# Kernel tuning notes

Hardware: AMD Instinct MI355X
Metric: run time of the kernel (lower is better)

The kernel has to match this reference:

```python
import jax, jax.numpy as jnp
import numpy as np
import math

D_MODEL = 1024
N_HEADS = 16
HEAD_DIM = D_MODEL // N_HEADS
B = 2
S = 2048

def setup_inputs() -> dict:
    key = jax.random.key(0)
    ks = jax.random.split(key, 5)
    x = jax.random.normal(ks[0], (B, S, D_MODEL), dtype=jnp.float32)
    # causal lower-triangular mask, broadcastable to [B, H, S, S]
    mask = jnp.tril(jnp.ones((S, S), dtype=bool))[None, None, :, :]
    # qkv_proj: Linear(d_model, 3*d_model); out_proj: Linear(d_model, d_model)
    lim_qkv = 1.0 / math.sqrt(D_MODEL)
    Wqkv = jax.random.uniform(ks[1], (D_MODEL, 3 * D_MODEL), minval=-lim_qkv, maxval=lim_qkv, dtype=jnp.float32)
    bqkv = jax.random.uniform(ks[2], (3 * D_MODEL,), minval=-lim_qkv, maxval=lim_qkv, dtype=jnp.float32)
    Wo = jax.random.uniform(ks[3], (D_MODEL, D_MODEL), minval=-lim_qkv, maxval=lim_qkv, dtype=jnp.float32)
    bo = jax.random.uniform(ks[4], (D_MODEL,), minval=-lim_qkv, maxval=lim_qkv, dtype=jnp.float32)
    return {"x": x, "mask": mask, "Wqkv": Wqkv, "bqkv": bqkv, "Wo": Wo, "bo": bo}

def reference(x, mask, Wqkv, bqkv, Wo, bo):
    b, s, d = x.shape
    scale = math.sqrt(HEAD_DIM)
    qkv = x @ Wqkv + bqkv                                   # [b, s, 3d]
    qkv = qkv.reshape(b, s, 3, N_HEADS, HEAD_DIM)
    qkv = jnp.transpose(qkv, (2, 0, 3, 1, 4))               # [3, b, h, s, hd]
    q, k, v = qkv[0], qkv[1], qkv[2]
    scores = jnp.einsum("bhqd,bhkd->bhqk", q, k) / scale    # [b, h, s, s]
    scores = jnp.where(mask, scores, -jnp.inf)
    attn = jax.nn.softmax(scores, axis=-1)                  # dropout inactive (eval)
    out = jnp.einsum("bhqk,bhkd->bhqd", attn, v)            # [b, h, s, hd]
    out = jnp.transpose(out, (0, 2, 1, 3)).reshape(b, s, d)
    return out @ Wo + bo
```

## Files before the change

kernel.cpp:

```cpp
#include <hip/hip_runtime.h>
#include <stdint.h>

typedef __bf16 bf16x8 __attribute__((ext_vector_type(8)));
typedef float  f32x4  __attribute__((ext_vector_type(4)));

__device__ __forceinline__ float bf2f(ushort u) {
    union { uint i; float f; } v; v.i = ((uint)u) << 16; return v.f;
}
__device__ __forceinline__ ushort f2bf(float f) {
    union { uint i; float f; } v; v.f = f;
    uint i = v.i;
    uint r = (i + 0x7fffu + ((i >> 16) & 1u)) >> 16;
    return (ushort)r;
}
__device__ __forceinline__ ushort f2bf_t(float f) {
    union { uint i; float f; } v; v.f = f;
    return (ushort)(v.i >> 16);
}

#if __has_builtin(__builtin_amdgcn_exp2f)
#define EXP2F __builtin_amdgcn_exp2f
#else
#define EXP2F exp2f
#endif

__device__ __forceinline__ void gld16(const ushort* g, ushort* l) {
    __builtin_amdgcn_global_load_lds((const __attribute__((address_space(1))) uint*)g,
                                     (__attribute__((address_space(3))) uint*)l, 16, 0, 0);
}

#define D_MODEL 1024
#define N_HEADS 16
#define HEAD_DIM 64
#define BATCH 2
#define SEQ 2048
#define M_ROWS (BATCH * SEQ)
#define N_ITEMS 1024
#define SCALE_LOG2E 0.18033688f

__global__ __launch_bounds__(256) void cast_f32_bf16(
    const float* __restrict__ in, ushort* __restrict__ out, int n4)
{
    int i = blockIdx.x * 256 + threadIdx.x;
    if (i < n4) {
        float4 v = ((const float4*)in)[i];
        ushort4 o;
        o.x = f2bf(v.x); o.y = f2bf(v.y); o.z = f2bf(v.z); o.w = f2bf(v.w);
        ((ushort4*)out)[i] = o;
    }
}

__global__ __launch_bounds__(256) void transpose_f32_bf16(
    const float* __restrict__ in, ushort* __restrict__ out, int K, int N)
{
    __shared__ float tile[64][65];
    const int k0 = blockIdx.y << 6, n0 = blockIdx.x << 6;
    const int tid = threadIdx.x;
    {
        const int r  = tid >> 4;
        const int c4 = (tid & 15) * 4;
#pragma unroll
        for (int rr = 0; rr < 4; ++rr) {
            int kk = r + rr * 16;
            float4 v = *(const float4*)(in + (size_t)(k0 + kk) * N + n0 + c4);
            tile[kk][c4 + 0] = v.x; tile[kk][c4 + 1] = v.y;
            tile[kk][c4 + 2] = v.z; tile[kk][c4 + 3] = v.w;
        }
    }
    __syncthreads();
    {
        const int nn = tid & 63;
        const int ch = tid >> 6;
#pragma unroll
        for (int cc = 0; cc < 2; ++cc) {
            int k8 = (ch + cc * 4) * 8;
            ushort tmp[8] __attribute__((aligned(16)));
#pragma unroll
            for (int j = 0; j < 8; ++j) tmp[j] = f2bf(tile[k8 + j][nn]);
            *(uint4*)(out + (size_t)(n0 + nn) * K + k0 + k8) = *(const uint4*)tmp;
        }
    }
}

__global__ __launch_bounds__(256) void gemm_bt128(
    const ushort* __restrict__ A, const ushort* __restrict__ Bt,
    const float* __restrict__ bias, float* __restrict__ out,
    ushort* __restrict__ Qb, ushort* __restrict__ Kb, ushort* __restrict__ Vb,
    int M, int N, int K, int mode)
{
    __shared__ ushort smem[64 * 136];
    ushort* As = smem;
    ushort* Bs = smem + 128 * 32;
    const int tid = threadIdx.x, lane = tid & 63, w = tid >> 6;
    const int wr = w >> 1, wc = w & 1;
    const int m0 = blockIdx.y * 128, n0 = blockIdx.x * 128;
    const int quad = lane >> 4, r15 = lane & 15, q8 = quad * 8;

    f32x4 acc[4][4] = {};

    const int cb0 = w * 64;
    const int cb1 = 256 + w * 64;
    const int c0 = cb0 + lane, c1 = cb1 + lane;
    const int row0 = c0 >> 2, sc0 = (c0 & 3) * 8;
    const int row1 = c1 >> 2, sc1 = (c1 & 3) * 8;

    for (int k0 = 0; k0 < K; k0 += 32) {
        gld16(A  + (size_t)(m0 + row0) * K + k0 + sc0, As + cb0 * 8);
        gld16(A  + (size_t)(m0 + row1) * K + k0 + sc1, As + cb1 * 8);
        gld16(Bt + (size_t)(n0 + row0) * K + k0 + sc0, Bs + cb0 * 8);
        gld16(Bt + (size_t)(n0 + row1) * K + k0 + sc1, Bs + cb1 * 8);
        __syncthreads();
        bf16x8 af[4], bfv[4];
#pragma unroll
        for (int mt = 0; mt < 4; ++mt)
            af[mt] = *(const bf16x8*)&As[(wr * 64 + mt * 16 + r15) * 32 + q8];
#pragma unroll
        for (int nt = 0; nt < 4; ++nt)
            bfv[nt] = *(const bf16x8*)&Bs[(wc * 64 + nt * 16 + r15) * 32 + q8];
#pragma unroll
        for (int mt = 0; mt < 4; ++mt)
#pragma unroll
            for (int nt = 0; nt < 4; ++nt)
                acc[mt][nt] = __builtin_amdgcn_mfma_f32_16x16x32_bf16(af[mt], bfv[nt], acc[mt][nt], 0, 0, 0);
        __syncthreads();
    }

    const int q4 = quad * 4;
    float bv[4];
#pragma unroll
    for (int nt = 0; nt < 4; ++nt) bv[nt] = bias[n0 + wc * 64 + nt * 16 + r15];

    if (mode == 0) {
        ushort* Cs = smem;
#pragma unroll
        for (int h = 0; h < 2; ++h) {
            __syncthreads();
            if (wr == h) {
#pragma unroll
                for (int mt = 0; mt < 4; ++mt)
#pragma unroll
                    for (int nt = 0; nt < 4; ++nt)
#pragma unroll
                        for (int r = 0; r < 4; ++r)
                            Cs[(mt * 16 + q4 + r) * 136 + wc * 64 + nt * 16 + r15] =
                                f2bf(acc[mt][nt][r] + bv[nt]);
            }
            __syncthreads();
#pragma unroll
            for (int it = 0; it < 4; ++it) {
                int idx = it * 256 + tid;
                int row = idx >> 4, chunk = idx & 15;
                int m = m0 + h * 64 + row;
                int n = n0 + chunk * 8;
                int which = n >> 10, nh = n & 1023;
                int hh = nh >> 6, d = nh & 63;
                int b = m >> 11, s = m & 2047;
                size_t dst = (((size_t)(b * N_HEADS + hh)) * SEQ + s) * HEAD_DIM + d;
                ushort* p = (which == 0) ? Qb : ((which == 1) ? Kb : Vb);
                *(uint4*)(p + dst) = *(const uint4*)&Cs[row * 136 + chunk * 8];
            }
        }
    } else {
#pragma unroll
        for (int mt = 0; mt < 4; ++mt) {
#pragma unroll
            for (int nt = 0; nt < 4; ++nt) {
#pragma unroll
                for (int r = 0; r < 4; ++r) {
                    int m = m0 + wr * 64 + mt * 16 + q4 + r;
                    int n = n0 + wc * 64 + nt * 16 + r15;
                    out[(size_t)m * N + n] = acc[mt][nt][r] + bv[nt];
                }
            }
        }
    }
}

__global__ __launch_bounds__(256) void attn_mfma(
    const ushort* __restrict__ Q, const ushort* __restrict__ K,
    const ushort* __restrict__ V, ushort* __restrict__ Out,
    int* __restrict__ counter)
{
    __shared__ ushort Ks[2][64 * 72];
    __shared__ ushort Vt[2][64 * 72];
    __shared__ ushort Ps[4][16 * 68];
    __shared__ int s_item;

    const int tid  = threadIdx.x;
    const int lane = tid & 63;
    const int w    = tid >> 6;
    const int quad = lane >> 4;
    const int r15  = lane & 15;
    const int q8   = quad * 8;

    const int srow = tid >> 2;
    const int scol = (tid & 3) * 16;
    const int kp = tid & 31;
    const int dg = tid >> 5;

    for (;;) {
        __syncthreads();
        if (tid == 0) s_item = atomicAdd(counter, 1);
        __syncthreads();
        const int item = s_item;
        if (item >= N_ITEMS) break;

        const int qblk = 31 - (item >> 5);
        const int bh   = item & 31;
        const int q0   = qblk * 64;
        const size_t base = (size_t)bh * SEQ * HEAD_DIM;
        const int wq0  = q0 + w * 16;
        const int ntiles = qblk + 1;

        bf16x8 qf[2];
        {
            const ushort* qrow = Q + base + (size_t)(wq0 + r15) * HEAD_DIM;
            qf[0] = *(const bf16x8*)(qrow + q8);
            qf[1] = *(const bf16x8*)(qrow + 32 + q8);
        }

        f32x4 o_acc[4] = {};
        float l_lane[4] = {0.f, 0.f, 0.f, 0.f};

        uint4 kr0, kr1, vr0, vr1;
        {
            const ushort* kpt = K + base + (size_t)srow * HEAD_DIM + scol;
            kr0 = *(const uint4*)kpt; kr1 = *(const uint4*)(kpt + 8);
            const ushort* vpt = V + base + (size_t)(2 * kp) * HEAD_DIM + dg * 8;
            vr0 = *(const uint4*)vpt; vr1 = *(const uint4*)(vpt + HEAD_DIM);
        }
        {
            ushort* ks = &Ks[0][0];
            *(uint4*)&ks[srow * 72 + scol]     = kr0;
            *(uint4*)&ks[srow * 72 + scol + 8] = kr1;
            const ushort* a = (const ushort*)&vr0;
            const ushort* b = (const ushort*)&vr1;
            uint* vt32 = (uint*)&Vt[0][0];
#pragma unroll
            for (int j = 0; j < 8; ++j)
                vt32[(dg * 8 + j) * 36 + ((kp + 4 * dg) & 31)] = (uint)a[j] | ((uint)b[j] << 16);
        }
        if (ntiles > 1) {
            const ushort* kpt = K + base + (size_t)(64 + srow) * HEAD_DIM + scol;
            kr0 = *(const uint4*)kpt; kr1 = *(const uint4*)(kpt + 8);
            const ushort* vpt = V + base + (size_t)(64 + 2 * kp) * HEAD_DIM + dg * 8;
            vr0 = *(const uint4*)vpt; vr1 = *(const uint4*)(vpt + HEAD_DIM);
        }

        for (int t = 0; t < ntiles; ++t) {
            __syncthreads();
            if (t + 1 < ntiles) {
                const int b1 = (t + 1) & 1;
                ushort* ks = &Ks[b1][0];
                *(uint4*)&ks[srow * 72 + scol]     = kr0;
                *(uint4*)&ks[srow * 72 + scol + 8] = kr1;
                const ushort* a = (const ushort*)&vr0;
                const ushort* b = (const ushort*)&vr1;
                uint* vt32 = (uint*)&Vt[b1][0];
#pragma unroll
                for (int j = 0; j < 8; ++j)
                    vt32[(dg * 8 + j) * 36 + ((kp + 4 * dg) & 31)] = (uint)a[j] | ((uint)b[j] << 16);
            }
            if (t + 2 < ntiles) {
                const int key2 = (t + 2) << 6;
                const ushort* kpt = K + base + (size_t)(key2 + srow) * HEAD_DIM + scol;
                kr0 = *(const uint4*)kpt; kr1 = *(const uint4*)(kpt + 8);
                const ushort* vpt = V + base + (size_t)(key2 + 2 * kp) * HEAD_DIM + dg * 8;
                vr0 = *(const uint4*)vpt; vr1 = *(const uint4*)(vpt + HEAD_DIM);
            }

            const ushort* KsB = &Ks[t & 1][0];
            const ushort* VtB = &Vt[t & 1][0];
            const bool diag = (t == ntiles - 1);
            const int ntmax = diag ? (w + 1) : 4;

            f32x4 s_acc[4];
            __builtin_amdgcn_s_setprio(1);
#pragma unroll
            for (int nt = 0; nt < 4; ++nt) {
                if (nt >= ntmax) continue;
                f32x4 z = {};
#pragma unroll
                for (int ks = 0; ks < 2; ++ks) {
                    bf16x8 kf = *(const bf16x8*)&KsB[(nt * 16 + r15) * 72 + ks * 32 + q8];
                    z = __builtin_amdgcn_mfma_f32_16x16x32_bf16(qf[ks], kf, z, 0, 0, 0);
                }
                s_acc[nt] = z;
            }
            __builtin_amdgcn_s_setprio(0);
#pragma unroll
            for (int nt = 0; nt < 4; ++nt) {
                if (nt >= ntmax) continue;
#pragma unroll
                for (int j = 0; j < 4; ++j) {
                    float e = EXP2F(s_acc[nt][j] * SCALE_LOG2E);
                    if (diag && nt == w && r15 > quad * 4 + j) e = 0.f;
                    s_acc[nt][j] = e;
                    l_lane[j] += e;
                }
            }
            ushort* pb = &Ps[w][0];
#pragma unroll
            for (int nt = 0; nt < 4; ++nt)
#pragma unroll
                for (int j = 0; j < 4; ++j)
                    pb[(quad * 4 + j) * 68 + nt * 16 + r15] =
                        (nt < ntmax) ? f2bf_t(s_acc[nt][j]) : (ushort)0;
            bf16x8 pf0 = *(const bf16x8*)&pb[r15 * 68 + q8];
            bf16x8 pf1 = *(const bf16x8*)&pb[r15 * 68 + 32 + q8];

            __builtin_amdgcn_s_setprio(1);
#pragma unroll
            for (int nt = 0; nt < 4; ++nt) {
                const int d0 = nt * 16 + r15;
                const int dsw = 4 * ((d0 >> 3) & 7);
                const int c0 = (4 * quad + dsw) & 31;
                const int c1 = (16 + 4 * quad + dsw) & 31;
                bf16x8 vf0 = *(const bf16x8*)&VtB[d0 * 72 + (c0 << 1)];
                bf16x8 vf1 = *(const bf16x8*)&VtB[d0 * 72 + (c1 << 1)];
                o_acc[nt] = __builtin_amdgcn_mfma_f32_16x16x32_bf16(pf0, vf0, o_acc[nt], 0, 0, 0);
                o_acc[nt] = __builtin_amdgcn_mfma_f32_16x16x32_bf16(pf1, vf1, o_acc[nt], 0, 0, 0);
            }
            __builtin_amdgcn_s_setprio(0);
        }

        float l_f[4];
#pragma unroll
        for (int j = 0; j < 4; ++j) {
            float l = l_lane[j];
            l += __shfl_xor(l, 1);
            l += __shfl_xor(l, 2);
            l += __shfl_xor(l, 4);
            l += __shfl_xor(l, 8);
            l_f[j] = 1.f / l;
        }
        const int b = bh >> 4, h = bh & 15;
#pragma unroll
        for (int nt = 0; nt < 4; ++nt) {
#pragma unroll
            for (int j = 0; j < 4; ++j) {
                int qg = wq0 + quad * 4 + j;
                float v = o_acc[nt][j] * l_f[j];
                Out[((size_t)(b * SEQ + qg)) * D_MODEL + h * 64 + nt * 16 + r15] = f2bf(v);
            }
        }
    }
}

extern "C" void kernel_launch(void* const* d_in, const int* in_sizes, int n_in,
                              void* d_out, int out_size, void* d_ws, size_t ws_size,
                              hipStream_t stream)
{
    const float* x    = (const float*)d_in[0];
    const float* Wqkv = (const float*)d_in[2];
    const float* bqkv = (const float*)d_in[3];
    const float* Wo   = (const float*)d_in[4];
    const float* bo   = (const float*)d_in[5];
    float* out = (float*)d_out;

    char* ws = (char*)d_ws;
    size_t off = 0;
    ushort* xb    = (ushort*)(ws + off); off += (size_t)M_ROWS * D_MODEL * 2;
    ushort* WqkvT = (ushort*)(ws + off); off += (size_t)3 * D_MODEL * D_MODEL * 2;
    ushort* WoT   = (ushort*)(ws + off); off += (size_t)D_MODEL * D_MODEL * 2;
    const size_t qkv_elems = (size_t)BATCH * N_HEADS * SEQ * HEAD_DIM;
    ushort* Qb = (ushort*)(ws + off); off += qkv_elems * 2;
    ushort* Kb = (ushort*)(ws + off); off += qkv_elems * 2;
    ushort* Vb = (ushort*)(ws + off); off += qkv_elems * 2;
    ushort* attn_out = (ushort*)(ws + off); off += (size_t)M_ROWS * D_MODEL * 2;
    int* counter = (int*)(ws + off); off += 256;

    hipMemsetAsync(counter, 0, 4, stream);

    {
        int n4 = M_ROWS * D_MODEL / 4;
        cast_f32_bf16<<<(n4 + 255) / 256, 256, 0, stream>>>(x, xb, n4);
    }

    transpose_f32_bf16<<<dim3(3 * D_MODEL / 64, D_MODEL / 64), 256, 0, stream>>>(Wqkv, WqkvT, D_MODEL, 3 * D_MODEL);
    transpose_f32_bf16<<<dim3(D_MODEL / 64, D_MODEL / 64), 256, 0, stream>>>(Wo, WoT, D_MODEL, D_MODEL);

    gemm_bt128<<<dim3(3 * D_MODEL / 128, M_ROWS / 128), 256, 0, stream>>>(
        xb, WqkvT, bqkv, nullptr, Qb, Kb, Vb, M_ROWS, 3 * D_MODEL, D_MODEL, 0);

    attn_mfma<<<768, 256, 0, stream>>>(Qb, Kb, Vb, attn_out, counter);

    gemm_bt128<<<dim3(D_MODEL / 128, M_ROWS / 128), 256, 0, stream>>>(
        attn_out, WoT, bo, out, nullptr, nullptr, nullptr, M_ROWS, D_MODEL, D_MODEL, 1);
}
```

Baseline: 231.1 us.

## Split long causal attention rows across two work items with combine pass

```diff
diff --git a/kernel.cpp b/kernel.cpp
--- a/kernel.cpp
+++ b/kernel.cpp
@@ -35,7 +35,6 @@
 #define BATCH 2
 #define SEQ 2048
 #define M_ROWS (BATCH * SEQ)
-#define N_ITEMS 1024
 #define SCALE_LOG2E 0.18033688f
 
 __global__ __launch_bounds__(256) void cast_f32_bf16(
@@ -179,11 +178,12 @@
 __global__ __launch_bounds__(256) void attn_mfma(
     const ushort* __restrict__ Q, const ushort* __restrict__ K,
     const ushort* __restrict__ V, ushort* __restrict__ Out,
-    int* __restrict__ counter)
+    float* __restrict__ Opart, float* __restrict__ Lpart,
+    int* __restrict__ counter, int n_items, int split)
 {
     __shared__ ushort Ks[2][64 * 72];
     __shared__ ushort Vt[2][64 * 72];
-    __shared__ ushort Ps[4][16 * 68];
+    __shared__ ushort Ps[4][16 * 72];
     __shared__ int s_item;
 
     const int tid  = threadIdx.x;
@@ -203,14 +203,25 @@
         if (tid == 0) s_item = atomicAdd(counter, 1);
         __syncthreads();
         const int item = s_item;
-        if (item >= N_ITEMS) break;
-
-        const int qblk = 31 - (item >> 5);
-        const int bh   = item & 31;
+        if (item >= n_items) break;
+
+        const int bh = item & 31;
+        int qblk, part, nparts;
+        if (split) {
+            const int i = item >> 5;
+            if (i < 32) { qblk = 31 - (i >> 1); part = i & 1; nparts = 2; }
+            else        { qblk = 47 - i;        part = 0;     nparts = 1; }
+        } else {
+            qblk = 31 - (item >> 5); part = 0; nparts = 1;
+        }
+        const int ntiles = qblk + 1;
+        const int half = (nparts == 2) ? ((ntiles + 1) >> 1) : ntiles;
+        const int t0 = (part == 0) ? 0 : half;
+        const int t1 = (part == 0) ? half : ntiles;
+
         const int q0   = qblk * 64;
         const size_t base = (size_t)bh * SEQ * HEAD_DIM;
         const int wq0  = q0 + w * 16;
-        const int ntiles = qblk + 1;
 
         bf16x8 qf[2];
         {
@@ -224,32 +235,32 @@
 
         uint4 kr0, kr1, vr0, vr1;
         {
-            const ushort* kpt = K + base + (size_t)srow * HEAD_DIM + scol;
+            const ushort* kpt = K + base + (size_t)((t0 << 6) + srow) * HEAD_DIM + scol;
             kr0 = *(const uint4*)kpt; kr1 = *(const uint4*)(kpt + 8);
-            const ushort* vpt = V + base + (size_t)(2 * kp) * HEAD_DIM + dg * 8;
+            const ushort* vpt = V + base + (size_t)((t0 << 6) + 2 * kp) * HEAD_DIM + dg * 8;
             vr0 = *(const uint4*)vpt; vr1 = *(const uint4*)(vpt + HEAD_DIM);
         }
         {
-            ushort* ks = &Ks[0][0];
+            ushort* ks = &Ks[t0 & 1][0];
             *(uint4*)&ks[srow * 72 + scol]     = kr0;
             *(uint4*)&ks[srow * 72 + scol + 8] = kr1;
             const ushort* a = (const ushort*)&vr0;
             const ushort* b = (const ushort*)&vr1;
-            uint* vt32 = (uint*)&Vt[0][0];
+            uint* vt32 = (uint*)&Vt[t0 & 1][0];
 #pragma unroll
             for (int j = 0; j < 8; ++j)
                 vt32[(dg * 8 + j) * 36 + ((kp + 4 * dg) & 31)] = (uint)a[j] | ((uint)b[j] << 16);
         }
-        if (ntiles > 1) {
-            const ushort* kpt = K + base + (size_t)(64 + srow) * HEAD_DIM + scol;
+        if (t0 + 1 < t1) {
+            const ushort* kpt = K + base + (size_t)(((t0 + 1) << 6) + srow) * HEAD_DIM + scol;
             kr0 = *(const uint4*)kpt; kr1 = *(const uint4*)(kpt + 8);
-            const ushort* vpt = V + base + (size_t)(64 + 2 * kp) * HEAD_DIM + dg * 8;
+            const ushort* vpt = V + base + (size_t)(((t0 + 1) << 6) + 2 * kp) * HEAD_DIM + dg * 8;
             vr0 = *(const uint4*)vpt; vr1 = *(const uint4*)(vpt + HEAD_DIM);
         }
 
-        for (int t = 0; t < ntiles; ++t) {
+        for (int t = t0; t < t1; ++t) {
             __syncthreads();
-            if (t + 1 < ntiles) {
+            if (t + 1 < t1) {
                 const int b1 = (t + 1) & 1;
                 ushort* ks = &Ks[b1][0];
                 *(uint4*)&ks[srow * 72 + scol]     = kr0;
@@ -261,7 +272,7 @@
                 for (int j = 0; j < 8; ++j)
                     vt32[(dg * 8 + j) * 36 + ((kp + 4 * dg) & 31)] = (uint)a[j] | ((uint)b[j] << 16);
             }
-            if (t + 2 < ntiles) {
+            if (t + 2 < t1) {
                 const int key2 = (t + 2) << 6;
                 const ushort* kpt = K + base + (size_t)(key2 + srow) * HEAD_DIM + scol;
                 kr0 = *(const uint4*)kpt; kr1 = *(const uint4*)(kpt + 8);
@@ -304,10 +315,10 @@
             for (int nt = 0; nt < 4; ++nt)
 #pragma unroll
                 for (int j = 0; j < 4; ++j)
-                    pb[(quad * 4 + j) * 68 + nt * 16 + r15] =
+                    pb[(quad * 4 + j) * 72 + nt * 16 + r15] =
                         (nt < ntmax) ? f2bf_t(s_acc[nt][j]) : (ushort)0;
-            bf16x8 pf0 = *(const bf16x8*)&pb[r15 * 68 + q8];
-            bf16x8 pf1 = *(const bf16x8*)&pb[r15 * 68 + 32 + q8];
+            bf16x8 pf0 = *(const bf16x8*)&pb[r15 * 72 + q8];
+            bf16x8 pf1 = *(const bf16x8*)&pb[r15 * 72 + 32 + q8];
 
             __builtin_amdgcn_s_setprio(1);
 #pragma unroll
@@ -324,7 +335,7 @@
             __builtin_amdgcn_s_setprio(0);
         }
 
-        float l_f[4];
+        float l_red[4];
 #pragma unroll
         for (int j = 0; j < 4; ++j) {
             float l = l_lane[j];
@@ -332,18 +343,64 @@
             l += __shfl_xor(l, 2);
             l += __shfl_xor(l, 4);
             l += __shfl_xor(l, 8);
-            l_f[j] = 1.f / l;
-        }
-        const int b = bh >> 4, h = bh & 15;
-#pragma unroll
-        for (int nt = 0; nt < 4; ++nt) {
-#pragma unroll
-            for (int j = 0; j < 4; ++j) {
-                int qg = wq0 + quad * 4 + j;
-                float v = o_acc[nt][j] * l_f[j];
-                Out[((size_t)(b * SEQ + qg)) * D_MODEL + h * 64 + nt * 16 + r15] = f2bf(v);
-            }
-        }
+            l_red[j] = l;
+        }
+        if (nparts == 2) {
+            const int slot = ((bh << 4) + (qblk - 16)) * 2 + part;
+            float* Op = Opart + (size_t)slot * 4096;
+            float* Lp = Lpart + (size_t)slot * 64;
+            const int rbase = w * 16 + quad * 4;
+            if (r15 == 0) {
+#pragma unroll
+                for (int j = 0; j < 4; ++j) Lp[rbase + j] = l_red[j];
+            }
+#pragma unroll
+            for (int nt = 0; nt < 4; ++nt)
+#pragma unroll
+                for (int j = 0; j < 4; ++j)
+                    Op[(rbase + j) * 64 + nt * 16 + r15] = o_acc[nt][j];
+        } else {
+            const int b = bh >> 4, h = bh & 15;
+#pragma unroll
+            for (int nt = 0; nt < 4; ++nt) {
+#pragma unroll
+                for (int j = 0; j < 4; ++j) {
+                    int qg = wq0 + quad * 4 + j;
+                    float v = o_acc[nt][j] / l_red[j];
+                    Out[((size_t)(b * SEQ + qg)) * D_MODEL + h * 64 + nt * 16 + r15] = f2bf(v);
+                }
+            }
+        }
+    }
+}
+
+__global__ __launch_bounds__(256) void attn_combine(
+    const float* __restrict__ Opart, const float* __restrict__ Lpart,
+    ushort* __restrict__ Out)
+{
+    const int sp = blockIdx.x;
+    const int bh = sp >> 4, qb16 = sp & 15;
+    const int qblk = 16 + qb16;
+    const int b = bh >> 4, h = bh & 15;
+    const float* O0 = Opart + (size_t)(sp * 2 + 0) * 4096;
+    const float* O1 = Opart + (size_t)(sp * 2 + 1) * 4096;
+    const float* L0 = Lpart + (size_t)(sp * 2 + 0) * 64;
+    const float* L1 = Lpart + (size_t)(sp * 2 + 1) * 64;
+    const int tid = threadIdx.x;
+#pragma unroll
+    for (int c = 0; c < 4; ++c) {
+        int e = c * 1024 + tid * 4;
+        int row = e >> 6, d = e & 63;
+        float4 a = *(const float4*)(O0 + e);
+        float4 bb = *(const float4*)(O1 + e);
+        float li = 1.f / (L0[row] + L1[row]);
+        ushort4 o;
+        o.x = f2bf((a.x + bb.x) * li);
+        o.y = f2bf((a.y + bb.y) * li);
+        o.z = f2bf((a.z + bb.z) * li);
+        o.w = f2bf((a.w + bb.w) * li);
+        int qg = qblk * 64 + row;
+        *(ushort4*)&Out[((size_t)(b * SEQ + qg)) * D_MODEL + h * 64 + d] = o;
     }
 }
 
@@ -369,6 +426,10 @@
     ushort* Vb = (ushort*)(ws + off); off += qkv_elems * 2;
     ushort* attn_out = (ushort*)(ws + off); off += (size_t)M_ROWS * D_MODEL * 2;
     int* counter = (int*)(ws + off); off += 256;
+    float* Opart = (float*)(ws + off); off += (size_t)32 * 16 * 2 * 4096 * 4;
+    float* Lpart = (float*)(ws + off); off += (size_t)32 * 16 * 2 * 64 * 4;
+    const int split = (off <= ws_size) ? 1 : 0;
+    const int n_items = split ? 1536 : 1024;
 
     hipMemsetAsync(counter, 0, 4, stream);
 
@@ -383,7 +444,10 @@
     gemm_bt128<<<dim3(3 * D_MODEL / 128, M_ROWS / 128), 256, 0, stream>>>(
         xb, WqkvT, bqkv, nullptr, Qb, Kb, Vb, M_ROWS, 3 * D_MODEL, D_MODEL, 0);
 
-    attn_mfma<<<768, 256, 0, stream>>>(Qb, Kb, Vb, attn_out, counter);
+    attn_mfma<<<768, 256, 0, stream>>>(Qb, Kb, Vb, attn_out, Opart, Lpart,
+                                       counter, n_items, split);
+    if (split)
+        attn_combine<<<512, 256, 0, stream>>>(Opart, Lpart, attn_out);
 
     gemm_bt128<<<dim3(D_MODEL / 128, M_ROWS / 128), 256, 0, stream>>>(
         attn_out, WoT, bo, out, nullptr, nullptr, nullptr, M_ROWS, D_MODEL, D_MODEL, 1);
```

Result: slower. 237.7 us (+2.9%).
